# Performance work log

Measured on AMD Instinct MI355X. Metric: run time of the kernel, lower is better.

Reference implementation:

```python
import jax, jax.numpy as jnp
import numpy as np
from jax import lax

K = 11  # AvgPool kernel
PAD = 5
EPS = 1e-5


def _box_avg(x):
    # Separable 11x11 box filter, stride 1, zero padding (count_include_pad=True)
    # x: [B, C, H, W]
    s = lax.reduce_window(x, 0.0, lax.add, (1, 1, K, 1), (1, 1, 1, 1),
                          [(0, 0), (0, 0), (PAD, PAD), (0, 0)])
    s = lax.reduce_window(s, 0.0, lax.add, (1, 1, 1, K), (1, 1, 1, 1),
                          [(0, 0), (0, 0), (0, 0), (PAD, PAD)])
    return s * (1.0 / (K * K))


def _bn(x, g, b, m, v):
    # eval-mode BatchNorm2d over channel dim (axis 1)
    scale = (g / jnp.sqrt(v + EPS))[None, :, None, None]
    shift = (b - m * g / jnp.sqrt(v + EPS))[None, :, None, None]
    return x * scale + shift


def setup_inputs() -> dict:
    key = jax.random.key(0)
    ks = jax.random.split(key, 13)
    B, C, H, W = 16, 256, 128, 128
    Ch = C // 2
    return {
        "x": jax.random.normal(ks[0], (B, C, H, W), jnp.float32),
        "w1": jax.random.normal(ks[1], (Ch, C), jnp.float32) * (1.0 / np.sqrt(C)),
        "b1": jax.random.normal(ks[2], (Ch,), jnp.float32) * 0.1,
        "bn1_g": jax.random.uniform(ks[3], (Ch,), jnp.float32, 0.5, 1.5),
        "bn1_b": jax.random.normal(ks[4], (Ch,), jnp.float32) * 0.1,
        "bn1_m": jax.random.normal(ks[5], (Ch,), jnp.float32) * 0.1,
        "bn1_v": jax.random.uniform(ks[6], (Ch,), jnp.float32, 0.5, 1.5),
        "w2": jax.random.normal(ks[7], (C, Ch), jnp.float32) * (1.0 / np.sqrt(Ch)),
        "b2": jax.random.normal(ks[8], (C,), jnp.float32) * 0.1,
        "bn2_g": jax.random.uniform(ks[9], (C,), jnp.float32, 0.5, 1.5),
        "bn2_b": jax.random.normal(ks[10], (C,), jnp.float32) * 0.1,
        "bn2_m": jax.random.normal(ks[11], (C,), jnp.float32) * 0.1,
        "bn2_v": jax.random.uniform(ks[12], (C,), jnp.float32, 0.5, 1.5),
    }


def reference(x, w1, b1, bn1_g, bn1_b, bn1_m, bn1_v,
              w2, b2, bn2_g, bn2_b, bn2_m, bn2_v):
    # edge features: high-pass via box-filter subtraction
    edge = x - _box_avg(x)
    # 1x1 conv -> BN -> ReLU
    h = jnp.einsum('bchw,oc->bohw', edge, w1) + b1[None, :, None, None]
    h = jax.nn.relu(_bn(h, bn1_g, bn1_b, bn1_m, bn1_v))
    # 1x1 conv -> BN -> Sigmoid
    w = jnp.einsum('bchw,oc->bohw', h, w2) + b2[None, :, None, None]
    w = jax.nn.sigmoid(_bn(w, bn2_g, bn2_b, bn2_m, bn2_v))
    # gated residual enhancement
    return w * x + x
```

## Files before the change

kernel.cpp:

```cpp
#include <hip/hip_runtime.h>

#define BB 16
#define CC 256
#define CH 128
#define HH 128
#define WW 128
#define HW (HH*WW)
#define KPOOL 11
#define PADP 5
#define EPS 1e-5f

typedef __attribute__((ext_vector_type(8))) short s16x8;
typedef __attribute__((ext_vector_type(4))) float f32x4;
typedef __attribute__((ext_vector_type(8))) unsigned short u16x8;
typedef __attribute__((ext_vector_type(4))) unsigned short u16x4;
typedef __attribute__((ext_vector_type(4))) unsigned int u32x4;

static __device__ __forceinline__ unsigned short f2bf(float f) {
    unsigned int u = __float_as_uint(f);
    u = u + 0x7fffu + ((u >> 16) & 1u);
    return (unsigned short)(u >> 16);
}
static __device__ __forceinline__ float bf2f(unsigned short h) {
    return __uint_as_float(((unsigned int)h) << 16);
}

#define MFMA16(a, b, c) __builtin_amdgcn_mfma_f32_16x16x32_bf16((a), (b), (c), 0, 0, 0)

__global__ __launch_bounds__(256) void prep_kernel(
    const float* __restrict__ w1, const float* __restrict__ b1,
    const float* __restrict__ g1, const float* __restrict__ be1,
    const float* __restrict__ m1, const float* __restrict__ v1,
    const float* __restrict__ w2, const float* __restrict__ b2,
    const float* __restrict__ g2, const float* __restrict__ be2,
    const float* __restrict__ m2, const float* __restrict__ v2,
    unsigned short* __restrict__ w1h, unsigned short* __restrict__ w1l,
    unsigned short* __restrict__ w2h, unsigned short* __restrict__ w2l,
    float* __restrict__ A1, float* __restrict__ B1,
    float* __restrict__ A2, float* __restrict__ B2)
{
    int i = blockIdx.x * 256 + threadIdx.x;
    if (i < CH * CC) {
        float w = w1[i];
        unsigned short hi = f2bf(w);
        w1h[i] = hi;
        w1l[i] = f2bf(w - bf2f(hi));
        float u = w2[i];
        unsigned short hi2 = f2bf(u);
        w2h[i] = hi2;
        w2l[i] = f2bf(u - bf2f(hi2));
    }
    if (i < CH) {
        float sc = g1[i] * rsqrtf(v1[i] + EPS);
        A1[i] = sc;
        B1[i] = be1[i] + (b1[i] - m1[i]) * sc;
    }
    if (i < CC) {
        float sc = g2[i] * rsqrtf(v2[i] + EPS);
        A2[i] = sc;
        B2[i] = be2[i] + (b2[i] - m2[i]) * sc;
    }
}

__global__ __launch_bounds__(256) void box_edge_kernel(
    const float* __restrict__ x, unsigned short* __restrict__ edge)
{
    constexpr int RB = 16;
    int blk  = blockIdx.x;
    int band = blk & 7;
    int bc   = blk >> 3;
    const float* img = x + (size_t)bc * HW;

    __shared__ float tile[RB + 2*PADP][WW];
    __shared__ float vs[RB][WW];
    __shared__ float P[RB][WW + 4];

    int h0 = band * RB;
    int t  = threadIdx.x;

    for (int idx = t; idx < (RB + 2*PADP) * (WW/4); idx += 256) {
        int r  = idx >> 5;
        int w4 = idx & 31;
        int h  = h0 - PADP + r;
        f32x4 v = {0.f, 0.f, 0.f, 0.f};
        if (h >= 0 && h < HH) v = *(const f32x4*)(img + h * WW + w4 * 4);
        *(f32x4*)&tile[r][w4 * 4] = v;
    }
    __syncthreads();

    {
        int w = t & 127, half = t >> 7;
        int r0 = half * 8;
        float s = 0.f;
#pragma unroll
        for (int j = 0; j < KPOOL; ++j) s += tile[r0 + j][w];
        vs[r0][w] = s;
#pragma unroll
        for (int k = 1; k < 8; ++k) {
            s += tile[r0 + 10 + k][w] - tile[r0 + k - 1][w];
            vs[r0 + k][w] = s;
        }
    }
    __syncthreads();

    {
        int lane = t & 63, wv = t >> 6;
#pragma unroll
        for (int rr = 0; rr < 4; ++rr) {
            int r = wv * 4 + rr;
            float v = vs[r][lane];
#pragma unroll
            for (int d = 1; d < 64; d <<= 1) {
                float u = __shfl_up(v, d, 64);
                if (lane >= d) v += u;
            }
            P[r][lane + 1] = v;
            float carry = __shfl(v, 63, 64);
            float v2 = vs[r][64 + lane];
#pragma unroll
            for (int d = 1; d < 64; d <<= 1) {
                float u = __shfl_up(v2, d, 64);
                if (lane >= d) v2 += u;
            }
            P[r][65 + lane] = v2 + carry;
            if (lane == 0) P[r][0] = 0.f;
        }
    }
    __syncthreads();

    for (int idx = t; idx < RB * WW; idx += 256) {
        int r = idx >> 7, w = idx & 127;
        int a = w - 5; if (a < 0) a = 0;
        int bq = w + 6; if (bq > 128) bq = 128;
        float s = P[r][bq] - P[r][a];
        float e = tile[r + PADP][w] - s * (1.f / (KPOOL * KPOOL));
        edge[(size_t)bc * HW + (size_t)(h0 + r) * WW + w] = f2bf(e);
    }
}

__global__ __launch_bounds__(256) void transpose_kernel(
    const unsigned short* __restrict__ edge_raw, unsigned short* __restrict__ edge_t)
{
    int blk = blockIdx.x;
    int c0 = (blk & 3) * 64;
    int p0 = ((blk >> 2) & 255) * 64;
    int b  = blk >> 10;

    __shared__ unsigned int lds32[64 * 33];

    int t  = threadIdx.x;
    int rp = t >> 3;
    int sl = t & 7;

    size_t rowA = ((size_t)(b * CC + c0 + 2 * rp)) << 14;
    u16x8 a = *(const u16x8*)(edge_raw + rowA + p0 + sl * 8);
    u16x8 c = *(const u16x8*)(edge_raw + rowA + (1 << 14) + p0 + sl * 8);

#pragma unroll
    for (int j = 0; j < 8; ++j) {
        unsigned int w = (unsigned int)a[j] | ((unsigned int)c[j] << 16);
        lds32[(sl * 8 + j) * 33 + rp] = w;
    }
    __syncthreads();

    int p = t >> 2;
    int q = t & 3;
    u32x4 o0, o1;
#pragma unroll
    for (int k = 0; k < 4; ++k) o0[k] = lds32[p * 33 + q * 8 + k];
#pragma unroll
    for (int k = 0; k < 4; ++k) o1[k] = lds32[p * 33 + q * 8 + 4 + k];

    unsigned short* dst = edge_t + (((size_t)(b * HW + p0 + p)) << 8) + c0 + q * 16;
    *(u32x4*)dst       = o0;
    *(u32x4*)(dst + 8) = o1;
}

__global__ __launch_bounds__(512, 6) void gemm12_fused(
    const unsigned short* __restrict__ edge_t,
    const unsigned short* __restrict__ w1h, const unsigned short* __restrict__ w1l,
    const float* __restrict__ A1, const float* __restrict__ B1,
    const unsigned short* __restrict__ w2h, const unsigned short* __restrict__ w2l,
    const float* __restrict__ A2, const float* __restrict__ B2,
    const float* __restrict__ x, float* __restrict__ out)
{
    const int blk  = blockIdx.x;
    const int b    = blk >> 8;
    const int p0   = (blk & 255) * 64;
    const int tid  = threadIdx.x;
    const int lane = tid & 63;
    const int l15  = lane & 15;
    const int l4   = lane >> 4;
    const int wv   = tid >> 6;

    __shared__ unsigned short hT[64 * 128];

    const unsigned short* E = edge_t + (((size_t)(b * HW + p0)) << 8);

    const f32x4 z4 = {0.f, 0.f, 0.f, 0.f};

    {
        const int o = wv * 16 + l15;
        f32x4 acc[4];
#pragma unroll
        for (int fp = 0; fp < 4; ++fp) acc[fp] = z4;

#pragma unroll
        for (int ks = 0; ks < 8; ++ks) {
            s16x8 bfr[4];
#pragma unroll
            for (int fp = 0; fp < 4; ++fp) {
                int pl = fp * 16 + l15;
                bfr[fp] = *(const s16x8*)(E + ((size_t)pl << 8) + ks * 32 + l4 * 8);
            }
            size_t wo = (size_t)o * CC + ks * 32 + l4 * 8;
            s16x8 ah = *(const s16x8*)(w1h + wo);
            s16x8 al = *(const s16x8*)(w1l + wo);
#pragma unroll
            for (int fp = 0; fp < 4; ++fp) {
                acc[fp] = MFMA16(ah, bfr[fp], acc[fp]);
                acc[fp] = MFMA16(al, bfr[fp], acc[fp]);
            }
        }

        int ob = wv * 16 + l4 * 4;
        f32x4 sc = *(const f32x4*)(A1 + ob);
        f32x4 sh = *(const f32x4*)(B1 + ob);
#pragma unroll
        for (int fp = 0; fp < 4; ++fp) {
            int pl = fp * 16 + l15;
            u16x4 hv;
#pragma unroll
            for (int r = 0; r < 4; ++r) {
                float v = acc[fp][r] * sc[r] + sh[r];
                v = fmaxf(v, 0.f);
                hv[r] = f2bf(v);
            }
            *(u16x4*)&hT[pl * 128 + ((ob >> 3) ^ (pl & 7)) * 8 + (ob & 7)] = hv;
        }
    }
    __syncthreads();

    {
        const int o0 = wv * 32;
        f32x4 acc[2][4];
#pragma unroll
        for (int fo = 0; fo < 2; ++fo)
#pragma unroll
            for (int fp = 0; fp < 4; ++fp) acc[fo][fp] = z4;

#pragma unroll
        for (int ks = 0; ks < 4; ++ks) {
            s16x8 bfr[4];
#pragma unroll
            for (int fp = 0; fp < 4; ++fp) {
                int pl = fp * 16 + l15;
                bfr[fp] = *(const s16x8*)&hT[pl * 128 + ((ks * 4 + l4) ^ (pl & 7)) * 8];
            }
#pragma unroll
            for (int fo = 0; fo < 2; ++fo) {
                int o = o0 + fo * 16 + l15;
                size_t wo = (size_t)o * CH + ks * 32 + l4 * 8;
                s16x8 ah = *(const s16x8*)(w2h + wo);
                s16x8 al = *(const s16x8*)(w2l + wo);
#pragma unroll
                for (int fp = 0; fp < 4; ++fp) {
                    acc[fo][fp] = MFMA16(ah, bfr[fp], acc[fo][fp]);
                    acc[fo][fp] = MFMA16(al, bfr[fp], acc[fo][fp]);
                }
            }
        }

#pragma unroll
        for (int fo = 0; fo < 2; ++fo) {
            int ob = o0 + fo * 16 + l4 * 4;
            f32x4 sc = *(const f32x4*)(A2 + ob);
            f32x4 sh = *(const f32x4*)(B2 + ob);
#pragma unroll
            for (int fp = 0; fp < 4; ++fp) {
                int p = p0 + fp * 16 + l15;
#pragma unroll
                for (int r = 0; r < 4; ++r) {
                    float z = acc[fo][fp][r] * sc[r] + sh[r];
                    float gte = 1.f / (1.f + __expf(-z));
                    size_t idx = (((size_t)(b * CC + ob + r)) << 14) + p;
                    out[idx] = x[idx] * (1.f + gte);
                }
            }
        }
    }
}

extern "C" void kernel_launch(void* const* d_in, const int* in_sizes, int n_in,
                              void* d_out, int out_size, void* d_ws, size_t ws_size,
                              hipStream_t stream) {
    const float* x   = (const float*)d_in[0];
    const float* w1  = (const float*)d_in[1];
    const float* b1  = (const float*)d_in[2];
    const float* g1  = (const float*)d_in[3];
    const float* be1 = (const float*)d_in[4];
    const float* m1  = (const float*)d_in[5];
    const float* v1  = (const float*)d_in[6];
    const float* w2  = (const float*)d_in[7];
    const float* b2  = (const float*)d_in[8];
    const float* g2  = (const float*)d_in[9];
    const float* be2 = (const float*)d_in[10];
    const float* m2  = (const float*)d_in[11];
    const float* v2  = (const float*)d_in[12];
    float* out = (float*)d_out;

    const size_t EDGE_BYTES  = (size_t)BB * CC * HW * 2;
    const size_t SMALL_BYTES = 4 * (size_t)CH * CC * 2 + (2 * CH + 2 * CC) * 4;

    unsigned short* edge_raw = (unsigned short*)d_out;
    unsigned short* edge_t;
    char* smalls;
    if (ws_size >= EDGE_BYTES + SMALL_BYTES) {
        edge_t = (unsigned short*)d_ws;
        smalls = (char*)d_ws + EDGE_BYTES;
    } else {
        edge_t = (unsigned short*)((char*)d_out + EDGE_BYTES);
        smalls = (char*)d_ws;
    }
    unsigned short* w1h = (unsigned short*)smalls;
    unsigned short* w1l = w1h + CH * CC;
    unsigned short* w2h = w1l + CH * CC;
    unsigned short* w2l = w2h + CH * CC;
    float* A1v = (float*)(w2l + CH * CC);
    float* B1v = A1v + CH;
    float* A2v = B1v + CH;
    float* B2v = A2v + CC;

    prep_kernel<<<128, 256, 0, stream>>>(w1, b1, g1, be1, m1, v1,
                                         w2, b2, g2, be2, m2, v2,
                                         w1h, w1l, w2h, w2l, A1v, B1v, A2v, B2v);

    box_edge_kernel<<<BB * CC * (HH / 16), 256, 0, stream>>>(x, edge_raw);

    transpose_kernel<<<BB * (HW / 64) * (CC / 64), 256, 0, stream>>>(edge_raw, edge_t);

    gemm12_fused<<<BB * (HW / 64), 512, 0, stream>>>(
        edge_t, w1h, w1l, A1v, B1v, w2h, w2l, A2v, B2v, x, out);
}
```

Before: 888.0 us.

## Stage edge tile in LDS, prefetch W1 fragments, and preload x before GEMM2

```diff
diff --git a/kernel.cpp b/kernel.cpp
--- a/kernel.cpp
+++ b/kernel.cpp
@@ -193,34 +193,54 @@
     const int l4   = lane >> 4;
     const int wv   = tid >> 6;
 
+    __shared__ unsigned short eT[64 * 256];
     __shared__ unsigned short hT[64 * 128];
 
     const unsigned short* E = edge_t + (((size_t)(b * HW + p0)) << 8);
+
+#pragma unroll
+    for (int i = 0; i < 4; ++i) {
+        int L  = i * 512 + tid;
+        int pl = L >> 5;
+        int s  = L & 31;
+        int g  = s ^ (pl & 7);
+        *(u16x8*)&eT[pl * 256 + s * 8] = *(const u16x8*)(E + pl * 256 + g * 8);
+    }
+    __syncthreads();
 
     const f32x4 z4 = {0.f, 0.f, 0.f, 0.f};
 
     {
         const int o = wv * 16 + l15;
+        const unsigned short* W1h = w1h + (size_t)o * CC;
+        const unsigned short* W1l = w1l + (size_t)o * CC;
+
         f32x4 acc[4];
 #pragma unroll
         for (int fp = 0; fp < 4; ++fp) acc[fp] = z4;
 
+        s16x8 ah = *(const s16x8*)(W1h + l4 * 8);
+        s16x8 al = *(const s16x8*)(W1l + l4 * 8);
+
 #pragma unroll
         for (int ks = 0; ks < 8; ++ks) {
+            s16x8 ah_n, al_n;
+            if (ks < 7) {
+                ah_n = *(const s16x8*)(W1h + (ks + 1) * 32 + l4 * 8);
+                al_n = *(const s16x8*)(W1l + (ks + 1) * 32 + l4 * 8);
+            }
             s16x8 bfr[4];
 #pragma unroll
             for (int fp = 0; fp < 4; ++fp) {
                 int pl = fp * 16 + l15;
-                bfr[fp] = *(const s16x8*)(E + ((size_t)pl << 8) + ks * 32 + l4 * 8);
-            }
-            size_t wo = (size_t)o * CC + ks * 32 + l4 * 8;
-            s16x8 ah = *(const s16x8*)(w1h + wo);
-            s16x8 al = *(const s16x8*)(w1l + wo);
+                bfr[fp] = *(const s16x8*)&eT[pl * 256 + ((ks * 4 + l4) ^ (pl & 7)) * 8];
+            }
 #pragma unroll
             for (int fp = 0; fp < 4; ++fp) {
                 acc[fp] = MFMA16(ah, bfr[fp], acc[fp]);
                 acc[fp] = MFMA16(al, bfr[fp], acc[fp]);
             }
+            ah = ah_n; al = al_n;
         }
 
         int ob = wv * 16 + l4 * 4;
@@ -243,6 +263,20 @@
 
     {
         const int o0 = wv * 32;
+
+        float xv[2][4][4];
+#pragma unroll
+        for (int fo = 0; fo < 2; ++fo) {
+            int ob = o0 + fo * 16 + l4 * 4;
+#pragma unroll
+            for (int fp = 0; fp < 4; ++fp) {
+                int p = p0 + fp * 16 + l15;
+#pragma unroll
+                for (int r = 0; r < 4; ++r)
+                    xv[fo][fp][r] = x[(((size_t)(b * CC + ob + r)) << 14) + p];
+            }
+        }
+
         f32x4 acc[2][4];
 #pragma unroll
         for (int fo = 0; fo < 2; ++fo)
@@ -284,7 +318,7 @@
                     float z = acc[fo][fp][r] * sc[r] + sh[r];
                     float gte = 1.f / (1.f + __expf(-z));
                     size_t idx = (((size_t)(b * CC + ob + r)) << 14) + p;
-                    out[idx] = x[idx] * (1.f + gte);
+                    out[idx] = xv[fo][fp][r] * (1.f + gte);
                 }
             }
         }
```

Result: faster. 770.6 us (-13.2%).
